# Optimization experiments

Hardware: AMD Instinct MI355X
Metric: run time of the kernel (lower is better)

Reference implementation:

```python
import jax, jax.numpy as jnp
import numpy as np

B, T, E, H = 64, 577, 768, 64
GRID_H, GRID_W = 24, 24
NUM_PREFIX = 1
N = GRID_H * GRID_W  # 576 patches
EPS = 1e-5


def setup_inputs() -> dict:
    key = jax.random.key(0)
    ks = jax.random.split(key, 12)
    s = lambda k, shape, fan: jax.random.normal(k, shape, jnp.float32) / np.sqrt(fan)
    return {
        "x": jax.random.normal(ks[0], (B, T, E), jnp.float32),
        "w_q": s(ks[1], (E, H), E),
        "w_k": s(ks[2], (E, H), E),
        "w_v": s(ks[3], (E, H), E),
        "q_gamma": jnp.ones((H,), jnp.float32),
        "q_beta": jnp.zeros((H,), jnp.float32),
        "k_gamma": jnp.ones((H,), jnp.float32),
        "k_beta": jnp.zeros((H,), jnp.float32),
        "w_sigma": s(ks[4], (H, 2), H),
        "b_sigma": jnp.zeros((2,), jnp.float32),
        "w_alpha": s(ks[5], (H, 1), H),
        "b_alpha": jnp.zeros((1,), jnp.float32),
    }


def _layernorm(x, gamma, beta):
    mu = jnp.mean(x, axis=-1, keepdims=True)
    var = jnp.mean(jnp.square(x - mu), axis=-1, keepdims=True)
    return (x - mu) * jax.lax.rsqrt(var + EPS) * gamma + beta


def _grid_sq_dists():
    # coords[i] = (row, col) of patch i; squared coordinate differences [N, N]
    coords = jnp.stack(
        jnp.meshgrid(jnp.arange(GRID_H), jnp.arange(GRID_W), indexing="ij"), axis=-1
    ).reshape(N, 2).astype(jnp.float32)
    diff = coords[:, None, :] - coords[None, :, :]  # [N, N, 2]
    dy2 = jnp.square(diff[..., 0])  # row diff squared
    dx2 = jnp.square(diff[..., 1])  # col diff squared
    return dx2, dy2


def reference(x, w_q, w_k, w_v, q_gamma, q_beta, k_gamma, k_beta,
              w_sigma, b_sigma, w_alpha, b_alpha):
    q = _layernorm(x @ w_q, q_gamma, q_beta)  # [B, T, H]
    k = _layernorm(x @ w_k, k_gamma, k_beta)  # [B, T, H]
    v = x @ w_v                               # [B, T, H]

    sim = jnp.einsum("bqh,bkh->bqk", q, k)    # [B, T, T]

    q_nc = q[:, NUM_PREFIX:, :]               # [B, N, H]
    alpha = jax.nn.softplus(q_nc @ w_alpha + b_alpha)[..., 0]  # [B, N]
    sigma = jax.nn.sigmoid(q_nc @ w_sigma + b_sigma)           # [B, N, 2]
    sx = sigma[..., 0]  # [B, N]
    sy = sigma[..., 1]

    dx2, dy2 = _grid_sq_dists()  # [N, N] each
    # Gaussian decay bias: query-patch p controls sigma; [B, N, N]
    G = jnp.exp(
        -dx2[None] / (2.0 * jnp.square(sx)[:, :, None])
        - dy2[None] / (2.0 * jnp.square(sy)[:, :, None])
    )
    S = alpha[:, :, None] * G

    sim = sim.at[:, NUM_PREFIX:, NUM_PREFIX:].add(S)

    scale = jnp.sqrt(jnp.float32(H))
    attn = jax.nn.softmax(sim / scale, axis=-1)
    return attn @ v  # [B, T, H]
```

## Files before the change

kernel.cpp:

```cpp
#include <hip/hip_runtime.h>
#include <math.h>

#define B_ 64
#define T_ 577
#define E_ 768
#define H_ 64
#define N_ 576
#define GW_ 24

typedef float f32x4 __attribute__((ext_vector_type(4)));
typedef __bf16 bf16x8 __attribute__((ext_vector_type(8)));
typedef __bf16 bf16x4 __attribute__((ext_vector_type(4)));

__device__ inline void split_bf16(float f, __bf16& h, __bf16& l) {
  h = (__bf16)f;
  l = (__bf16)(f - (float)h);
}

__device__ inline float bperm_f(int byte_addr, float x) {
  return __int_as_float(__builtin_amdgcn_ds_bpermute(byte_addr, __float_as_int(x)));
}

__global__ __launch_bounds__(256) void prep_w_kernel(
    const float* __restrict__ wq, const float* __restrict__ wk, const float* __restrict__ wv,
    __bf16* __restrict__ wsw_hi, __bf16* __restrict__ wsw_lo)
{
  int t = blockIdx.x * 256 + threadIdx.x;
  if (t >= 24*192) return;
  int kc = t / 192, n = t - (t/192)*192;
  const float* src = (n < 64) ? wq : ((n < 128) ? wk : wv);
  int nn = n & 63;
  __bf16 hbuf[32], lbuf[32];
  #pragma unroll
  for (int kk = 0; kk < 32; ++kk) {
    float f = src[(size_t)(kc*32 + kk)*64 + nn];
    split_bf16(f, hbuf[kk], lbuf[kk]);
  }
  size_t base = (size_t)t * 32;
  #pragma unroll
  for (int i = 0; i < 4; ++i) {
    *(bf16x8*)(wsw_hi + base + i*8) = *(bf16x8*)&hbuf[i*8];
    *(bf16x8*)(wsw_lo + base + i*8) = *(bf16x8*)&lbuf[i*8];
  }
}

__global__ __launch_bounds__(256) void qkv_ln_kernel(
    const float* __restrict__ x,
    const __bf16* __restrict__ wsw_hi, const __bf16* __restrict__ wsw_lo,
    const float* __restrict__ qg, const float* __restrict__ qb,
    const float* __restrict__ kg, const float* __restrict__ kb,
    const float* __restrict__ wsig, const float* __restrict__ bsig,
    const float* __restrict__ walp, const float* __restrict__ balp,
    float* __restrict__ qo, float* __restrict__ ko, float* __restrict__ vo,
    float* __restrict__ alo, float* __restrict__ sxo, float* __restrict__ syo)
{
  __shared__ __align__(16) float smem[64*193 + 256];
  __bf16* A_hi = (__bf16*)smem;
  __bf16* A_lo = A_hi + 64*40;
  __bf16* B_hi = A_lo + 64*40;
  __bf16* B_lo = B_hi + 192*40;
  float (*Cs)[193] = (float (*)[193])smem;
  float* mu_q = smem + 64*193;
  float* rs_q = mu_q + 64;
  float* mu_k = rs_q + 64;
  float* rs_k = mu_k + 64;

  const int tid  = threadIdx.x;
  const int lane = tid & 63;
  const int w    = tid >> 6;
  const int rowbase = blockIdx.x << 6;

  f32x4 acc[4][3];
  #pragma unroll
  for (int mt = 0; mt < 4; ++mt)
    #pragma unroll
    for (int nt = 0; nt < 3; ++nt)
      acc[mt][nt] = (f32x4){0.f, 0.f, 0.f, 0.f};

  const int m     = lane & 15;
  const int kfrag = (lane >> 4) * 8;

  float4 xr0, xr1;
  bf16x8 whr[3], wlr[3];
  const int s0 = tid, s1 = tid + 256;
  const int arow0 = s0 >> 3, ak0 = (s0 & 7) * 4;
  const int arow1 = s1 >> 3, ak1 = (s1 & 7) * 4;

  auto load_chunk = [&](int kc) {
    xr0 = *(const float4*)(x + (size_t)(rowbase + arow0)*E_ + kc*32 + ak0);
    xr1 = *(const float4*)(x + (size_t)(rowbase + arow1)*E_ + kc*32 + ak1);
    #pragma unroll
    for (int i = 0; i < 3; ++i) {
      int e = tid + 256*i;
      whr[i] = *(const bf16x8*)(wsw_hi + (size_t)kc*6144 + e*8);
      wlr[i] = *(const bf16x8*)(wsw_lo + (size_t)kc*6144 + e*8);
    }
  };
  auto store_chunk = [&]() {
    __bf16 h0,l0,h1,l1,h2,l2,h3,l3;
    split_bf16(xr0.x,h0,l0); split_bf16(xr0.y,h1,l1);
    split_bf16(xr0.z,h2,l2); split_bf16(xr0.w,h3,l3);
    *(bf16x4*)&A_hi[arow0*40 + ak0] = (bf16x4){h0,h1,h2,h3};
    *(bf16x4*)&A_lo[arow0*40 + ak0] = (bf16x4){l0,l1,l2,l3};
    split_bf16(xr1.x,h0,l0); split_bf16(xr1.y,h1,l1);
    split_bf16(xr1.z,h2,l2); split_bf16(xr1.w,h3,l3);
    *(bf16x4*)&A_hi[arow1*40 + ak1] = (bf16x4){h0,h1,h2,h3};
    *(bf16x4*)&A_lo[arow1*40 + ak1] = (bf16x4){l0,l1,l2,l3};
    #pragma unroll
    for (int i = 0; i < 3; ++i) {
      int e = tid + 256*i;
      int n = e >> 2, g = e & 3;
      *(bf16x8*)&B_hi[n*40 + g*8] = whr[i];
      *(bf16x8*)&B_lo[n*40 + g*8] = wlr[i];
    }
  };

  load_chunk(0);
  #pragma unroll 1
  for (int kc = 0; kc < 24; ++kc) {
    __syncthreads();
    store_chunk();
    __syncthreads();
    if (kc < 23) load_chunk(kc + 1);

    bf16x8 bh[3], bl[3];
    #pragma unroll
    for (int nt = 0; nt < 3; ++nt) {
      int n = w*48 + nt*16 + m;
      bh[nt] = *(const bf16x8*)&B_hi[n*40 + kfrag];
      bl[nt] = *(const bf16x8*)&B_lo[n*40 + kfrag];
    }
    #pragma unroll
    for (int mt = 0; mt < 4; ++mt) {
      bf16x8 ah = *(const bf16x8*)&A_hi[(mt*16 + m)*40 + kfrag];
      bf16x8 al = *(const bf16x8*)&A_lo[(mt*16 + m)*40 + kfrag];
      #pragma unroll
      for (int nt = 0; nt < 3; ++nt) {
        acc[mt][nt] = __builtin_amdgcn_mfma_f32_16x16x32_bf16(ah, bh[nt], acc[mt][nt], 0, 0, 0);
        acc[mt][nt] = __builtin_amdgcn_mfma_f32_16x16x32_bf16(al, bh[nt], acc[mt][nt], 0, 0, 0);
        acc[mt][nt] = __builtin_amdgcn_mfma_f32_16x16x32_bf16(ah, bl[nt], acc[mt][nt], 0, 0, 0);
      }
    }
  }
  __syncthreads();

  #pragma unroll
  for (int mt = 0; mt < 4; ++mt)
    #pragma unroll
    for (int nt = 0; nt < 3; ++nt) {
      int row = mt*16 + (lane >> 4)*4;
      int col = w*48 + nt*16 + (lane & 15);
      Cs[row + 0][col] = acc[mt][nt].x;
      Cs[row + 1][col] = acc[mt][nt].y;
      Cs[row + 2][col] = acc[mt][nt].z;
      Cs[row + 3][col] = acc[mt][nt].w;
    }
  __syncthreads();

  if (tid < 64) {
    float s = 0.f;
    for (int h = 0; h < 64; ++h) s += Cs[tid][h];
    float mu = s * (1.f/64.f);
    float vs = 0.f;
    for (int h = 0; h < 64; ++h) { float d = Cs[tid][h] - mu; vs += d*d; }
    mu_q[tid] = mu;
    rs_q[tid] = rsqrtf(vs*(1.f/64.f) + 1e-5f);
  } else if (tid < 128) {
    int r = tid - 64;
    float s = 0.f;
    for (int h = 0; h < 64; ++h) s += Cs[r][64+h];
    float mu = s * (1.f/64.f);
    float vs = 0.f;
    for (int h = 0; h < 64; ++h) { float d = Cs[r][64+h] - mu; vs += d*d; }
    mu_k[r] = mu;
    rs_k[r] = rsqrtf(vs*(1.f/64.f) + 1e-5f);
  }
  __syncthreads();

  if (tid >= 192) {
    int r = tid - 192;
    int mrow = rowbase + r;
    int tindex = mrow % T_;
    if (tindex >= 1) {
      int bb = mrow / T_;
      int g = tindex - 1;
      float mu = mu_q[r], rs = rs_q[r];
      float za = 0.f, z0 = 0.f, z1 = 0.f;
      for (int h = 0; h < 64; ++h) {
        float qv = (Cs[r][h] - mu) * rs * qg[h] + qb[h];
        za += qv * walp[h];
        z0 += qv * wsig[2*h];
        z1 += qv * wsig[2*h+1];
      }
      za += balp[0]; z0 += bsig[0]; z1 += bsig[1];
      float al = fmaxf(za, 0.f) + log1pf(__expf(-fabsf(za)));
      float sx = 1.f/(1.f + __expf(-z0));
      float sy = 1.f/(1.f + __expf(-z1));
      alo[bb*N_ + g] = al;
      sxo[bb*N_ + g] = 0.5f/(sx*sx);
      syo[bb*N_ + g] = 0.5f/(sy*sy);
    }
  }
  for (int idx = tid; idx < 64*48; idx += 256) {
    int r = idx / 48, c4 = (idx - (idx/48)*48) * 4;
    size_t row = (size_t)rowbase + r;
    float4 val = make_float4(Cs[r][c4], Cs[r][c4+1], Cs[r][c4+2], Cs[r][c4+3]);
    if (c4 < 64) {
      float mu = mu_q[r], rs = rs_q[r];
      float4 o;
      o.x = (val.x - mu)*rs*qg[c4+0] + qb[c4+0];
      o.y = (val.y - mu)*rs*qg[c4+1] + qb[c4+1];
      o.z = (val.z - mu)*rs*qg[c4+2] + qb[c4+2];
      o.w = (val.w - mu)*rs*qg[c4+3] + qb[c4+3];
      *(float4*)(qo + row*64 + c4) = o;
    } else if (c4 < 128) {
      int h = c4 - 64;
      float mu = mu_k[r], rs = rs_k[r];
      float4 o;
      o.x = (val.x - mu)*rs*kg[h+0] + kb[h+0];
      o.y = (val.y - mu)*rs*kg[h+1] + kb[h+1];
      o.z = (val.z - mu)*rs*kg[h+2] + kb[h+2];
      o.w = (val.w - mu)*rs*kg[h+3] + kb[h+3];
      *(float4*)(ko + row*64 + h) = o;
    } else {
      *(float4*)(vo + row*64 + (c4-128)) = val;
    }
  }
}

__global__ __launch_bounds__(256, 4) void attn_kernel(
    const float* __restrict__ q, const float* __restrict__ k, const float* __restrict__ v,
    const float* __restrict__ ala, const float* __restrict__ sxa, const float* __restrict__ sya,
    float* __restrict__ out)
{
  __shared__ __align__(16) __bf16 sm[4*4608];
  __bf16* KH = sm;            __bf16* KL = sm + 4608;
  __bf16* VH = sm + 2*4608;   __bf16* VL = sm + 3*4608;

  const int tid  = threadIdx.x;
  const int lane = tid & 63;
  const int w    = tid >> 6;
  const int quad = lane >> 4;
  const int m    = lane & 15;

  const int f       = blockIdx.y * 10 + blockIdx.x;
  const int logical = (f & 7) * 80 + (f >> 3);
  const int b       = logical / 10;
  const int qt      = logical - b * 10;

  const float* qbase = q + (size_t)b * T_ * H_;
  const float* kbase = k + (size_t)b * T_ * H_;
  const float* vbase = v + (size_t)b * T_ * H_;

  const int  row    = qt*64 + w*16 + m;
  const int  rowc   = row < T_ ? row : T_ - 1;
  const bool qvalid = row < T_;
  const bool qhas   = (row >= 1) && qvalid;
  float al = 0.f, isx = 0.f, isy = 0.f, qr = 0.f, qc = 0.f;
  {
    int g = qhas ? row - 1 : 0;
    if (qhas) {
      al  = ala[b*N_ + g] * 0.125f;
      isx = sxa[b*N_ + g];
      isy = sya[b*N_ + g];
      int gr = g / GW_;
      qr = (float)gr;
      qc = (float)(g - gr*GW_);
    }
  }

  bf16x8 qh[2], ql[2];
  #pragma unroll
  for (int ks = 0; ks < 2; ++ks) {
    float4 f0 = *(const float4*)(qbase + (size_t)rowc*H_ + ks*32 + quad*8);
    float4 f1 = *(const float4*)(qbase + (size_t)rowc*H_ + ks*32 + quad*8 + 4);
    float fv[8] = {f0.x, f0.y, f0.z, f0.w, f1.x, f1.y, f1.z, f1.w};
    #pragma unroll
    for (int j = 0; j < 8; ++j) {
      float s = fv[j] * 0.125f;
      __bf16 h, l;
      split_bf16(s, h, l);
      qh[ks][j] = h;
      ql[ks][j] = l;
    }
  }

  float mo = -INFINITY, lsum = 0.f;
  f32x4 acc[4];
  #pragma unroll
  for (int nt = 0; nt < 4; ++nt) acc[nt] = (f32x4){0.f, 0.f, 0.f, 0.f};

  const int  addrA = ((2*(quad & 1))*16 + m) * 4;
  const int  addrB = addrA + 64;
  const bool hiNT  = quad >= 2;

  float4 kreg[4];
  float  vreg[16];
  const int d0 = tid & 15, k0 = (tid >> 4) * 4;

  auto load_kv = [&](int kt) {
    #pragma unroll
    for (int i = 0; i < 4; ++i) {
      int s = tid + 256*i;
      int key = s >> 4, c4 = (s & 15)*4;
      int kgl = kt*64 + key;
      int kcl = kgl < T_ ? kgl : T_ - 1;
      kreg[i] = *(const float4*)(kbase + (size_t)kcl*H_ + c4);
    }
    #pragma unroll
    for (int di = 0; di < 4; ++di)
      #pragma unroll
      for (int ki = 0; ki < 4; ++ki) {
        int kgl = kt*64 + k0 + ki;
        int kcl = kgl < T_ ? kgl : T_ - 1;
        vreg[di*4+ki] = vbase[(size_t)kcl*H_ + d0 + 16*di];
      }
  };
  auto store_kv = [&]() {
    #pragma unroll
    for (int i = 0; i < 4; ++i) {
      int s = tid + 256*i;
      int key = s >> 4, c4 = (s & 15)*4;
      __bf16 h0,l0,h1,l1,h2,l2,h3,l3;
      split_bf16(kreg[i].x,h0,l0); split_bf16(kreg[i].y,h1,l1);
      split_bf16(kreg[i].z,h2,l2); split_bf16(kreg[i].w,h3,l3);
      *(bf16x4*)&KH[key*72 + c4] = (bf16x4){h0,h1,h2,h3};
      *(bf16x4*)&KL[key*72 + c4] = (bf16x4){l0,l1,l2,l3};
    }
    #pragma unroll
    for (int di = 0; di < 4; ++di) {
      int dim = d0 + 16*di;
      __bf16 h0,l0,h1,l1,h2,l2,h3,l3;
      split_bf16(vreg[di*4+0],h0,l0); split_bf16(vreg[di*4+1],h1,l1);
      split_bf16(vreg[di*4+2],h2,l2); split_bf16(vreg[di*4+3],h3,l3);
      *(bf16x4*)&VH[dim*72 + k0] = (bf16x4){h0,h1,h2,h3};
      *(bf16x4*)&VL[dim*72 + k0] = (bf16x4){l0,l1,l2,l3};
    }
  };

  load_kv(0);
  #pragma unroll 1
  for (int kt = 0; kt < 10; ++kt) {
    __syncthreads();
    store_kv();
    __syncthreads();
    if (kt < 9) load_kv(kt + 1);

    float s_[4][4];
    #pragma unroll
    for (int nt = 0; nt < 4; ++nt) {
      f32x4 sac = (f32x4){0.f, 0.f, 0.f, 0.f};
      #pragma unroll
      for (int ks = 0; ks < 2; ++ks) {
        const int ko_ = ks*32 + quad*8;
        bf16x8 kh = *(const bf16x8*)&KH[(nt*16 + m)*72 + ko_];
        bf16x8 kl = *(const bf16x8*)&KL[(nt*16 + m)*72 + ko_];
        sac = __builtin_amdgcn_mfma_f32_16x16x32_bf16(kh, qh[ks], sac, 0, 0, 0);
        sac = __builtin_amdgcn_mfma_f32_16x16x32_bf16(kl, qh[ks], sac, 0, 0, 0);
        sac = __builtin_amdgcn_mfma_f32_16x16x32_bf16(kh, ql[ks], sac, 0, 0, 0);
      }
      s_[nt][0] = sac.x; s_[nt][1] = sac.y; s_[nt][2] = sac.z; s_[nt][3] = sac.w;
    }

    #pragma unroll
    for (int nt = 0; nt < 4; ++nt) {
      #pragma unroll
      for (int reg = 0; reg < 4; ++reg) {
        int key = kt*64 + nt*16 + quad*4 + reg;
        float sval = s_[nt][reg];
        float kgf = (float)(key - 1);
        float krf = floorf(kgf * (1.0f/24.0f));
        float kcf = kgf - 24.f*krf;
        float dx = qc - kcf, dy = qr - krf;
        float bias = al * __expf(-(dx*dx*isx + dy*dy*isy));
        bool khas = (key >= 1) && (key < T_);
        sval += (khas && qhas) ? bias : 0.f;
        s_[nt][reg] = (key < T_) ? sval : -1e30f;
      }
    }

    float mx = s_[0][0];
    #pragma unroll
    for (int nt = 0; nt < 4; ++nt)
      #pragma unroll
      for (int reg = 0; reg < 4; ++reg)
        mx = fmaxf(mx, s_[nt][reg]);
    mx = fmaxf(mx, __shfl_xor(mx, 16, 64));
    mx = fmaxf(mx, __shfl_xor(mx, 32, 64));
    float mn = fmaxf(mo, mx);
    float sc = __expf(mo - mn);
    float lt = 0.f;
    #pragma unroll
    for (int nt = 0; nt < 4; ++nt)
      #pragma unroll
      for (int reg = 0; reg < 4; ++reg) {
        float p = __expf(s_[nt][reg] - mn);
        s_[nt][reg] = p;
        lt += p;
      }
    lt += __shfl_xor(lt, 16, 64);
    lt += __shfl_xor(lt, 32, 64);
    lsum = lsum*sc + lt;
    mo = mn;
    #pragma unroll
    for (int nt = 0; nt < 4; ++nt) {
      acc[nt].x *= sc; acc[nt].y *= sc; acc[nt].z *= sc; acc[nt].w *= sc;
    }

    bf16x8 fh[2], fl[2];
    #pragma unroll
    for (int ks = 0; ks < 2; ++ks) {
      #pragma unroll
      for (int reg = 0; reg < 4; ++reg) {
        float xa0 = bperm_f(addrA, s_[2*ks+0][reg]);
        float xa1 = bperm_f(addrA, s_[2*ks+1][reg]);
        float xb0 = bperm_f(addrB, s_[2*ks+0][reg]);
        float xb1 = bperm_f(addrB, s_[2*ks+1][reg]);
        float va = hiNT ? xa1 : xa0;
        float vb = hiNT ? xb1 : xb0;
        __bf16 h, l;
        split_bf16(va, h, l); fh[ks][reg]   = h; fl[ks][reg]   = l;
        split_bf16(vb, h, l); fh[ks][4+reg] = h; fl[ks][4+reg] = l;
      }
    }

    #pragma unroll
    for (int nt = 0; nt < 4; ++nt) {
      f32x4 c = acc[nt];
      #pragma unroll
      for (int ks = 0; ks < 2; ++ks) {
        const int ko_ = ks*32 + quad*8;
        bf16x8 vh = *(const bf16x8*)&VH[(nt*16 + m)*72 + ko_];
        bf16x8 vl = *(const bf16x8*)&VL[(nt*16 + m)*72 + ko_];
        c = __builtin_amdgcn_mfma_f32_16x16x32_bf16(vh, fh[ks], c, 0, 0, 0);
        c = __builtin_amdgcn_mfma_f32_16x16x32_bf16(vl, fh[ks], c, 0, 0, 0);
        c = __builtin_amdgcn_mfma_f32_16x16x32_bf16(vh, fl[ks], c, 0, 0, 0);
      }
      acc[nt] = c;
    }
  }

  if (qvalid) {
    float inv = 1.f / lsum;
    #pragma unroll
    for (int nt = 0; nt < 4; ++nt) {
      float4 o;
      o.x = acc[nt].x * inv;
      o.y = acc[nt].y * inv;
      o.z = acc[nt].z * inv;
      o.w = acc[nt].w * inv;
      *(float4*)(out + ((size_t)b*T_ + row)*H_ + nt*16 + quad*4) = o;
    }
  }
}

extern "C" void kernel_launch(void* const* d_in, const int* in_sizes, int n_in,
                              void* d_out, int out_size, void* d_ws, size_t ws_size,
                              hipStream_t stream) {
  const float* x      = (const float*)d_in[0];
  const float* wq     = (const float*)d_in[1];
  const float* wk     = (const float*)d_in[2];
  const float* wv     = (const float*)d_in[3];
  const float* qg     = (const float*)d_in[4];
  const float* qb     = (const float*)d_in[5];
  const float* kg     = (const float*)d_in[6];
  const float* kb     = (const float*)d_in[7];
  const float* wsig   = (const float*)d_in[8];
  const float* bsig   = (const float*)d_in[9];
  const float* walp   = (const float*)d_in[10];
  const float* balp   = (const float*)d_in[11];
  float* out = (float*)d_out;

  float* ws  = (float*)d_ws;
  const size_t nrow = (size_t)B_ * T_;
  float* qo  = ws;
  float* ko  = qo + nrow*H_;
  float* vo  = ko + nrow*H_;
  float* alo = vo + nrow*H_;
  float* sxo = alo + (size_t)B_*N_;
  float* syo = sxo + (size_t)B_*N_;
  __bf16* wsw_hi = (__bf16*)(syo + (size_t)B_*N_);
  __bf16* wsw_lo = wsw_hi + 24*192*32;

  hipLaunchKernelGGL(prep_w_kernel, dim3(18), dim3(256), 0, stream,
                     wq, wk, wv, wsw_hi, wsw_lo);
  hipLaunchKernelGGL(qkv_ln_kernel, dim3(577), dim3(256), 0, stream,
                     x, wsw_hi, wsw_lo, qg, qb, kg, kb, wsig, bsig, walp, balp,
                     qo, ko, vo, alo, sxo, syo);
  hipLaunchKernelGGL(attn_kernel, dim3(10, B_), dim3(256), 0, stream,
                     qo, ko, vo, alo, sxo, syo, out);
}
```

Baseline: 289.9 us.

## Stream weight tiles to LDS via async global_load_lds with double buffering

The QKV projection kernel now copies the pre-split bf16 weight chunks straight from global memory into LDS with global_load_lds, double-buffered across K chunks. This removes the register staging and the explicit LDS stores for the B operand. The prep kernel writes a combined hi/lo layout with an XOR swizzle that the reader undoes, to avoid LDS bank conflicts without padding. In exchange the kernel uses more LDS per block, which may lower occupancy, and correctness depends on the async loads finishing before the next barrier.

```diff
diff --git a/kernel.cpp b/kernel.cpp
--- a/kernel.cpp
+++ b/kernel.cpp
@@ -21,32 +21,38 @@
   return __int_as_float(__builtin_amdgcn_ds_bpermute(byte_addr, __float_as_int(x)));
 }
 
+#define GLOAD_LDS16(G, L)                                                     \
+  __builtin_amdgcn_global_load_lds(                                           \
+      (const __attribute__((address_space(1))) void*)(G),                     \
+      (__attribute__((address_space(3))) void*)(L), 16, 0, 0)
+
 __global__ __launch_bounds__(256) void prep_w_kernel(
     const float* __restrict__ wq, const float* __restrict__ wk, const float* __restrict__ wv,
-    __bf16* __restrict__ wsw_hi, __bf16* __restrict__ wsw_lo)
+    __bf16* __restrict__ wsw2)
 {
   int t = blockIdx.x * 256 + threadIdx.x;
   if (t >= 24*192) return;
-  int kc = t / 192, n = t - (t/192)*192;
+  int kc = t / 192, n = t - kc*192;
   const float* src = (n < 64) ? wq : ((n < 128) ? wk : wv);
   int nn = n & 63;
-  __bf16 hbuf[32], lbuf[32];
+  int xb = (n & 3) ^ ((n >> 2) & 3);
+  size_t cbase = (size_t)kc * 12288;
   #pragma unroll
-  for (int kk = 0; kk < 32; ++kk) {
-    float f = src[(size_t)(kc*32 + kk)*64 + nn];
-    split_bf16(f, hbuf[kk], lbuf[kk]);
-  }
-  size_t base = (size_t)t * 32;
-  #pragma unroll
-  for (int i = 0; i < 4; ++i) {
-    *(bf16x8*)(wsw_hi + base + i*8) = *(bf16x8*)&hbuf[i*8];
-    *(bf16x8*)(wsw_lo + base + i*8) = *(bf16x8*)&lbuf[i*8];
+  for (int g = 0; g < 4; ++g) {
+    __bf16 hb[8], lb[8];
+    #pragma unroll
+    for (int j = 0; j < 8; ++j) {
+      float f = src[(size_t)(kc*32 + g*8 + j)*64 + nn];
+      split_bf16(f, hb[j], lb[j]);
+    }
+    int slot = n*4 + (g ^ xb);
+    *(bf16x8*)(wsw2 + cbase + slot*8)        = *(bf16x8*)hb;
+    *(bf16x8*)(wsw2 + cbase + 6144 + slot*8) = *(bf16x8*)lb;
   }
 }
 
 __global__ __launch_bounds__(256) void qkv_ln_kernel(
-    const float* __restrict__ x,
-    const __bf16* __restrict__ wsw_hi, const __bf16* __restrict__ wsw_lo,
+    const float* __restrict__ x, const __bf16* __restrict__ wsw2,
     const float* __restrict__ qg, const float* __restrict__ qb,
     const float* __restrict__ kg, const float* __restrict__ kb,
     const float* __restrict__ wsig, const float* __restrict__ bsig,
@@ -54,11 +60,11 @@
     float* __restrict__ qo, float* __restrict__ ko, float* __restrict__ vo,
     float* __restrict__ alo, float* __restrict__ sxo, float* __restrict__ syo)
 {
-  __shared__ __align__(16) float smem[64*193 + 256];
+  __shared__ __align__(16) float smem[14848];
   __bf16* A_hi = (__bf16*)smem;
-  __bf16* A_lo = A_hi + 64*40;
-  __bf16* B_hi = A_lo + 64*40;
-  __bf16* B_lo = B_hi + 192*40;
+  __bf16* A_lo = A_hi + 2560;
+  __bf16* B0   = A_lo + 2560;
+  __bf16* B1   = B0 + 12288;
   float (*Cs)[193] = (float (*)[193])smem;
   float* mu_q = smem + 64*193;
   float* rs_q = mu_q + 64;
@@ -68,6 +74,8 @@
   const int tid  = threadIdx.x;
   const int lane = tid & 63;
   const int w    = tid >> 6;
+  const int quad = lane >> 4;
+  const int m    = lane & 15;
   const int rowbase = blockIdx.x << 6;
 
   f32x4 acc[4][3];
@@ -77,26 +85,18 @@
     for (int nt = 0; nt < 3; ++nt)
       acc[mt][nt] = (f32x4){0.f, 0.f, 0.f, 0.f};
 
-  const int m     = lane & 15;
-  const int kfrag = (lane >> 4) * 8;
+  const int kfrag = quad * 8;
+  const int xl    = quad ^ (m & 3) ^ (m >> 2);
 
   float4 xr0, xr1;
-  bf16x8 whr[3], wlr[3];
-  const int s0 = tid, s1 = tid + 256;
-  const int arow0 = s0 >> 3, ak0 = (s0 & 7) * 4;
-  const int arow1 = s1 >> 3, ak1 = (s1 & 7) * 4;
-
-  auto load_chunk = [&](int kc) {
+  const int arow0 = tid >> 3,        ak0 = (tid & 7) * 4;
+  const int arow1 = (tid + 256) >> 3, ak1 = (tid & 7) * 4;
+
+  auto load_A = [&](int kc) {
     xr0 = *(const float4*)(x + (size_t)(rowbase + arow0)*E_ + kc*32 + ak0);
     xr1 = *(const float4*)(x + (size_t)(rowbase + arow1)*E_ + kc*32 + ak1);
-    #pragma unroll
-    for (int i = 0; i < 3; ++i) {
-      int e = tid + 256*i;
-      whr[i] = *(const bf16x8*)(wsw_hi + (size_t)kc*6144 + e*8);
-      wlr[i] = *(const bf16x8*)(wsw_lo + (size_t)kc*6144 + e*8);
-    }
   };
-  auto store_chunk = [&]() {
+  auto store_A = [&]() {
     __bf16 h0,l0,h1,l1,h2,l2,h3,l3;
     split_bf16(xr0.x,h0,l0); split_bf16(xr0.y,h1,l1);
     split_bf16(xr0.z,h2,l2); split_bf16(xr0.w,h3,l3);
@@ -106,29 +106,35 @@
     split_bf16(xr1.z,h2,l2); split_bf16(xr1.w,h3,l3);
     *(bf16x4*)&A_hi[arow1*40 + ak1] = (bf16x4){h0,h1,h2,h3};
     *(bf16x4*)&A_lo[arow1*40 + ak1] = (bf16x4){l0,l1,l2,l3};
-    #pragma unroll
-    for (int i = 0; i < 3; ++i) {
-      int e = tid + 256*i;
-      int n = e >> 2, g = e & 3;
-      *(bf16x8*)&B_hi[n*40 + g*8] = whr[i];
-      *(bf16x8*)&B_lo[n*40 + g*8] = wlr[i];
-    }
   };
-
-  load_chunk(0);
+  auto issue_B = [&](int kc, __bf16* Bbuf) {
+    const __bf16* sbase = wsw2 + (size_t)kc*12288 + (size_t)(w*6)*512 + lane*8;
+    __bf16* dbase = Bbuf + (w*6)*512;
+    #pragma unroll
+    for (int j = 0; j < 6; ++j)
+      GLOAD_LDS16(sbase + j*512, dbase + j*512);
+  };
+
+  issue_B(0, B0);
+  load_A(0);
   #pragma unroll 1
   for (int kc = 0; kc < 24; ++kc) {
+    __bf16* Bcur = (kc & 1) ? B1 : B0;
+    __bf16* Bnxt = (kc & 1) ? B0 : B1;
     __syncthreads();
-    store_chunk();
+    store_A();
     __syncthreads();
-    if (kc < 23) load_chunk(kc + 1);
+    if (kc < 23) {
+      issue_B(kc + 1, Bnxt);
+      load_A(kc + 1);
+    }
 
     bf16x8 bh[3], bl[3];
     #pragma unroll
     for (int nt = 0; nt < 3; ++nt) {
-      int n = w*48 + nt*16 + m;
-      bh[nt] = *(const bf16x8*)&B_hi[n*40 + kfrag];
-      bl[nt] = *(const bf16x8*)&B_lo[n*40 + kfrag];
+      int slotb = (w*48 + nt*16 + m)*4 + xl;
+      bh[nt] = *(const bf16x8*)&Bcur[slotb*8];
+      bl[nt] = *(const bf16x8*)&Bcur[6144 + slotb*8];
     }
     #pragma unroll
     for (int mt = 0; mt < 4; ++mt) {
@@ -148,8 +154,8 @@
   for (int mt = 0; mt < 4; ++mt)
     #pragma unroll
     for (int nt = 0; nt < 3; ++nt) {
-      int row = mt*16 + (lane >> 4)*4;
-      int col = w*48 + nt*16 + (lane & 15);
+      int row = mt*16 + quad*4;
+      int col = w*48 + nt*16 + m;
       Cs[row + 0][col] = acc[mt][nt].x;
       Cs[row + 1][col] = acc[mt][nt].y;
       Cs[row + 2][col] = acc[mt][nt].z;
@@ -479,13 +485,12 @@
   float* alo = vo + nrow*H_;
   float* sxo = alo + (size_t)B_*N_;
   float* syo = sxo + (size_t)B_*N_;
-  __bf16* wsw_hi = (__bf16*)(syo + (size_t)B_*N_);
-  __bf16* wsw_lo = wsw_hi + 24*192*32;
+  __bf16* wsw2 = (__bf16*)(syo + (size_t)B_*N_);
 
   hipLaunchKernelGGL(prep_w_kernel, dim3(18), dim3(256), 0, stream,
-                     wq, wk, wv, wsw_hi, wsw_lo);
+                     wq, wk, wv, wsw2);
   hipLaunchKernelGGL(qkv_ln_kernel, dim3(577), dim3(256), 0, stream,
-                     x, wsw_hi, wsw_lo, qg, qb, kg, kb, wsig, bsig, walp, balp,
+                     x, wsw2, qg, qb, kg, kb, wsig, bsig, walp, balp,
                      qo, ko, vo, alo, sxo, syo);
   hipLaunchKernelGGL(attn_kernel, dim3(10, B_), dim3(256), 0, stream,
                      qo, ko, vo, alo, sxo, syo, out);
```

Result: slower. 305.9 us (+5.5%).
